# Optimization experiments

Hardware: AMD Instinct MI355X
Metric: run time of the kernel (lower is better)

The kernel has to match this reference:

```python
import jax, jax.numpy as jnp
import numpy as np

V, E, D = 100000, 128, 60  # vocab, embedding_size, d_alpha
B, J, M, P = 512, 101, 50, 5120
EPS = 1e-6


def setup_inputs() -> dict:
    key = jax.random.key(0)
    ks = jax.random.split(key, 12)
    s = 0.5 / E
    inp = {
        'batch_titems': jax.random.randint(ks[0], (B, J), 0, V),
        'batch_citems': jax.random.randint(ks[1], (B, M), 0, V),
        'batch_pad_ids': jax.random.randint(ks[2], (2, P), 0, M),
        't_emb': jax.random.uniform(ks[3], (V, E), jnp.float32, -s, s),
        'c_emb': jax.random.uniform(ks[4], (V, E), jnp.float32, -s, s),
        'Ac_w': jax.random.normal(ks[5], (D, E), jnp.float32) * 0.05,
        'Ac_b': jnp.zeros((D,), jnp.float32),
        'At_w': jax.random.normal(ks[6], (D, E), jnp.float32) * 0.05,
        'At_b': jnp.zeros((D,), jnp.float32),
        'Bc_w': jax.random.normal(ks[7], (E, E), jnp.float32) * 0.05,
        'Bc_b': jnp.zeros((E,), jnp.float32),
        'R_w': jax.random.normal(ks[8], (E, E), jnp.float32) * 0.05,
        'R_b': jnp.zeros((E,), jnp.float32),
    }
    return inp


def reference(batch_titems, batch_citems, batch_pad_ids, t_emb, c_emb,
              Ac_w, Ac_b, At_w, At_b, Bc_w, Bc_b, R_w, R_b):
    v = t_emb[batch_titems]            # [B, J, E] target item vectors
    u = c_emb[batch_citems]            # [B, M, E] context item vectors
    tp = v @ At_w.T + At_b             # [B, J, D]
    cp = u @ Ac_w.T + Ac_b             # [B, M, D]
    # cosine similarity with torch eps clamp on norms
    dot = jnp.einsum('bjd,bmd->bjm', tp, cp)
    nt = jnp.maximum(jnp.linalg.norm(tp, axis=-1), EPS)  # [B, J]
    nc = jnp.maximum(jnp.linalg.norm(cp, axis=-1), EPS)  # [B, M]
    cos = dot / (nt[:, :, None] * nc[:, None, :])        # [B, J, M]
    # pad mask: (batch, context-pos) pairs masked across all J target rows
    mask = jnp.zeros((cos.shape[0], cos.shape[2]), bool)
    mask = mask.at[batch_pad_ids[0], batch_pad_ids[1]].set(True)
    scores = jnp.where(mask[:, None, :], -jnp.inf, cos)
    attn = jax.nn.softmax(scores, axis=-1)               # [B, J, M]
    bu = u @ Bc_w.T + Bc_b                               # [B, M, E]
    alpha = jnp.einsum('bjm,bme->bje', attn, bu)         # [B, J, E]
    return alpha @ R_w.T + R_b                           # [B, J, E]
```

## Files before the change

### kernel.cpp

```cpp
#include <hip/hip_runtime.h>

typedef unsigned short u16;
typedef unsigned int   u32;
typedef short bf8 __attribute__((ext_vector_type(8)));
typedef float f4  __attribute__((ext_vector_type(4)));

#define NB   512
#define NJ   101
#define NM   50
#define NE   128
#define ND   60
#define NP   5120
#define NT   512
#define EPSV 1e-6f

#define T_B    0
#define C_B    16128
#define H_B    25344
#define NT2_B  43776
#define NC2_B  44224
#define MSK_B  44480
#define ARENA  44736

__device__ __forceinline__ u16 f2bh(float f) {
    return (u16)((__float_as_uint(f) + 0x8000u) >> 16);
}
__device__ __forceinline__ u32 pk2(float a, float b) {
    u32 ia = __float_as_uint(a) + 0x8000u;
    u32 ib = __float_as_uint(b) + 0x8000u;
    return (ia >> 16) | (ib & 0xFFFF0000u);
}
__device__ __forceinline__ bf8 pkfrag(float4 x, float4 y) {
    union { u32 u[4]; bf8 v; } r;
    r.u[0] = pk2(x.x, x.y); r.u[1] = pk2(x.z, x.w);
    r.u[2] = pk2(y.x, y.y); r.u[3] = pk2(y.z, y.w);
    return r.v;
}

__global__ __launch_bounds__(128) void w2_kernel(
    const float* __restrict__ Bc_w, const float* __restrict__ Bc_b,
    const float* __restrict__ R_w,  const float* __restrict__ R_b,
    const float* __restrict__ At_w, const float* __restrict__ Ac_w,
    u16* __restrict__ w2t, float* __restrict__ rb2,
    u16* __restrict__ atw, u16* __restrict__ acw)
{
    const int e = blockIdx.x, k = threadIdx.x;
    const float* Rrow = R_w + e * NE;
    float a0 = 0.f, a1 = 0.f, a2 = 0.f, a3 = 0.f;
    #pragma unroll 8
    for (int j = 0; j < NE; j += 4) {
        a0 += Rrow[j]     * Bc_w[j * NE + k];
        a1 += Rrow[j + 1] * Bc_w[(j + 1) * NE + k];
        a2 += Rrow[j + 2] * Bc_w[(j + 2) * NE + k];
        a3 += Rrow[j + 3] * Bc_w[(j + 3) * NE + k];
    }
    w2t[e * NE + k] = f2bh((a0 + a1) + (a2 + a3));
    if (e < ND) {
        atw[e * NE + k] = f2bh(At_w[e * NE + k]);
        acw[e * NE + k] = f2bh(Ac_w[e * NE + k]);
    }
    float c = Bc_b[k] * Rrow[k];
    for (int o = 32; o; o >>= 1) c += __shfl_xor(c, o, 64);
    __shared__ float part[2];
    if ((k & 63) == 0) part[k >> 6] = c;
    __syncthreads();
    if (k == 0) rb2[e] = part[0] + part[1] + R_b[e];
}

__device__ __forceinline__ void tp_full(int jt, int l15, int quad, const bf8* A,
    const u16* __restrict__ atw, const float* __restrict__ At_b,
    u16* __restrict__ tp16, float* __restrict__ nt2)
{
    #pragma unroll
    for (int dt = 0; dt < 4; dt++) {
        const int d = dt * 16 + l15;
        const u16* arow = atw + (size_t)((d < ND) ? d : 0) * NE;
        float bv = (d < ND) ? At_b[d] : 0.f;
        f4 acc = {bv, bv, bv, bv};
        #pragma unroll
        for (int ks = 0; ks < 4; ks++)
            acc = __builtin_amdgcn_mfma_f32_16x16x32_bf16(
                A[ks], *(const bf8*)(arow + ks * 32 + quad * 8), acc, 0, 0, 0);
        const int j0 = jt * 16 + quad * 4;
        #pragma unroll
        for (int r = 0; r < 4; r++) {
            float v = acc[r];
            tp16[(j0 + r) * 72 + d] = (d < ND) ? f2bh(v) : (u16)0;
            float q = (d < ND) ? v * v : 0.f;
            q += __shfl_xor(q, 1, 64); q += __shfl_xor(q, 2, 64);
            q += __shfl_xor(q, 4, 64); q += __shfl_xor(q, 8, 64);
            if (l15 == 0) atomicAdd(&nt2[j0 + r], q);
        }
    }
}

__device__ __forceinline__ void cp_full(int mt, int l15, int quad, const bf8* Au,
    const u16* __restrict__ acw, const float* __restrict__ Ac_b,
    u16* __restrict__ cp16, float* __restrict__ nc2)
{
    #pragma unroll
    for (int dt = 0; dt < 4; dt++) {
        const int d = dt * 16 + l15;
        const u16* arow = acw + (size_t)((d < ND) ? d : 0) * NE;
        float bv = (d < ND) ? Ac_b[d] : 0.f;
        f4 acc = {bv, bv, bv, bv};
        #pragma unroll
        for (int ks = 0; ks < 4; ks++)
            acc = __builtin_amdgcn_mfma_f32_16x16x32_bf16(
                Au[ks], *(const bf8*)(arow + ks * 32 + quad * 8), acc, 0, 0, 0);
        const int m0 = mt * 16 + quad * 4;
        #pragma unroll
        for (int r = 0; r < 4; r++) {
            float v = acc[r];
            cp16[(m0 + r) * 72 + d] = (d < ND) ? f2bh(v) : (u16)0;
            float q = (d < ND) ? v * v : 0.f;
            q += __shfl_xor(q, 1, 64); q += __shfl_xor(q, 2, 64);
            q += __shfl_xor(q, 4, 64); q += __shfl_xor(q, 8, 64);
            if (l15 == 0) atomicAdd(&nc2[m0 + r], q);
        }
    }
}

__device__ __forceinline__ void ht_group(int mtg, int l15, int quad, const bf8* Au,
    const u16* __restrict__ w2t, u16* __restrict__ hT16)
{
    #pragma unroll
    for (int et = 0; et < 8; et++) {
        const u16* wrow = w2t + (size_t)(et * 16 + l15) * NE;
        f4 acc = {0.f, 0.f, 0.f, 0.f};
        #pragma unroll
        for (int ks = 0; ks < 4; ks++)
            acc = __builtin_amdgcn_mfma_f32_16x16x32_bf16(
                *(const bf8*)(wrow + ks * 32 + quad * 8), Au[ks], acc, 0, 0, 0);
        const int e0 = et * 16 + quad * 4;
        #pragma unroll
        for (int r = 0; r < 4; r++)
            hT16[(e0 + r) * 72 + mtg * 16 + l15] = f2bh(acc[r]);
    }
}

__global__ __launch_bounds__(NT, 3) void aitv_kernel(
    const int* __restrict__ titems, const int* __restrict__ citems,
    const int* __restrict__ pad_ids,
    const float* __restrict__ t_emb, const float* __restrict__ c_emb,
    const u16* __restrict__ atw,     const float* __restrict__ At_b,
    const u16* __restrict__ acw,     const float* __restrict__ Ac_b,
    const u16* __restrict__ w2t,     const float* __restrict__ rb2g,
    float* __restrict__ out)
{
    const int b    = blockIdx.x;
    const int t    = threadIdx.x;
    const int wid  = t >> 6;
    const int lane = t & 63;
    const int l15  = lane & 15;
    const int quad = lane >> 4;

    __shared__ __align__(16) char arena[ARENA];
    u16*   tp16 = (u16*)(arena + T_B);   u16* at16 = (u16*)(arena + T_B);
    u16*   cp16 = (u16*)(arena + C_B);
    u16*   hT16 = (u16*)(arena + H_B);
    float* nt2  = (float*)(arena + NT2_B);
    float* nc2  = (float*)(arena + NC2_B);
    int*   msk  = (int*)(arena + MSK_B);

    float4 pxT[8];
    if (wid < 7) {
        int j = wid * 16 + l15; if (j > NJ - 1) j = NJ - 1;
        const float* vr = t_emb + (size_t)titems[b * NJ + j] * NE + quad * 8;
        #pragma unroll
        for (int h = 0; h < 8; h++)
            pxT[h] = *(const float4*)(vr + (h >> 1) * 32 + (h & 1) * 4);
    }
    const int mtu = (wid < 4) ? wid : wid - 4;
    int mrow = mtu * 16 + l15; if (mrow > NM - 1) mrow = NM - 1;
    const float* vrU = c_emb + (size_t)citems[b * NM + mrow] * NE + quad * 8;

    if (t < 112) nt2[t] = 0.f;
    else if (t < 176) nc2[t - 112] = 0.f;
    else if (t < 240) msk[t - 176] = 0;
    __syncthreads();

    float4 pxU[8];
    #pragma unroll
    for (int h = 0; h < 8; h++)
        pxU[h] = *(const float4*)(vrU + (h >> 1) * 32 + (h & 1) * 4);

    for (int i = t; i < NP; i += NT)
        if (pad_ids[i] == b) msk[pad_ids[NP + i]] = 1;

    bf8 At[4];
    if (wid < 7) {
        #pragma unroll
        for (int ks = 0; ks < 4; ks++) At[ks] = pkfrag(pxT[2 * ks], pxT[2 * ks + 1]);
        tp_full(wid, l15, quad, At, atw, At_b, tp16, nt2);
    }
    bf8 Au[4];
    #pragma unroll
    for (int ks = 0; ks < 4; ks++) Au[ks] = pkfrag(pxU[2 * ks], pxU[2 * ks + 1]);
    if (wid < 4) ht_group(mtu, l15, quad, Au, w2t, hT16);
    else         cp_full(mtu, l15, quad, Au, acw, Ac_b, cp16, nc2);
    __syncthreads();

    if (wid < 7) {
        const int jt = wid;
        f4 S[4];
        #pragma unroll
        for (int mt = 0; mt < 4; mt++) {
            f4 acc = {0.f, 0.f, 0.f, 0.f};
            #pragma unroll
            for (int ks = 0; ks < 2; ks++) {
                bf8 a  = *(const bf8*)(tp16 + (jt * 16 + l15) * 72 + ks * 32 + quad * 8);
                bf8 bb = *(const bf8*)(cp16 + (mt * 16 + l15) * 72 + ks * 32 + quad * 8);
                acc = __builtin_amdgcn_mfma_f32_16x16x32_bf16(a, bb, acc, 0, 0, 0);
            }
            S[mt] = acc;
        }
        bool valid[4]; float ncS[4];
        #pragma unroll
        for (int mt = 0; mt < 4; mt++) {
            int m = mt * 16 + l15;
            valid[mt] = (m < NM) && (msk[m] == 0);
            ncS[mt]   = valid[mt] ? fmaxf(sqrtf(nc2[m]), EPSV) : 1.f;
        }
        #pragma unroll
        for (int r = 0; r < 4; r++) {
            int j = jt * 16 + quad * 4 + r;
            float ntj = fmaxf(sqrtf(nt2[j]), EPSV);
            float x[4], mx = -INFINITY;
            #pragma unroll
            for (int mt = 0; mt < 4; mt++) {
                x[mt] = valid[mt] ? S[mt][r] / (ntj * ncS[mt]) : -INFINITY;
                mx = fmaxf(mx, x[mt]);
            }
            mx = fmaxf(mx, __shfl_xor(mx, 1, 64)); mx = fmaxf(mx, __shfl_xor(mx, 2, 64));
            mx = fmaxf(mx, __shfl_xor(mx, 4, 64)); mx = fmaxf(mx, __shfl_xor(mx, 8, 64));
            float p[4], sm = 0.f;
            #pragma unroll
            for (int mt = 0; mt < 4; mt++) {
                p[mt] = valid[mt] ? __expf(x[mt] - mx) : 0.f;
                sm += p[mt];
            }
            sm += __shfl_xor(sm, 1, 64); sm += __shfl_xor(sm, 2, 64);
            sm += __shfl_xor(sm, 4, 64); sm += __shfl_xor(sm, 8, 64);
            float inv = (sm > 0.f) ? 1.f / sm : 0.f;
            #pragma unroll
            for (int mt = 0; mt < 4; mt++)
                at16[j * 72 + mt * 16 + l15] = f2bh(p[mt] * inv);
        }
    }
    __syncthreads();

    for (int u = wid; u < 56; u += 8) {
        int jt = u >> 3, et = u & 7;
        float bv = rb2g[et * 16 + l15];
        f4 acc = {bv, bv, bv, bv};
        #pragma unroll
        for (int ks = 0; ks < 2; ks++) {
            bf8 a  = *(const bf8*)(at16 + (jt * 16 + l15) * 72 + ks * 32 + quad * 8);
            bf8 bb = *(const bf8*)(hT16 + (et * 16 + l15) * 72 + ks * 32 + quad * 8);
            acc = __builtin_amdgcn_mfma_f32_16x16x32_bf16(a, bb, acc, 0, 0, 0);
        }
        int e = et * 16 + l15, j0 = jt * 16 + quad * 4;
        #pragma unroll
        for (int r = 0; r < 4; r++) {
            int j = j0 + r;
            if (j < NJ) out[((size_t)b * NJ + j) * NE + e] = acc[r];
        }
    }
}

extern "C" void kernel_launch(void* const* d_in, const int* in_sizes, int n_in,
                              void* d_out, int out_size, void* d_ws, size_t ws_size,
                              hipStream_t stream) {
    const int*   titems  = (const int*)d_in[0];
    const int*   citems  = (const int*)d_in[1];
    const int*   pad_ids = (const int*)d_in[2];
    const float* t_emb   = (const float*)d_in[3];
    const float* c_emb   = (const float*)d_in[4];
    const float* Ac_w    = (const float*)d_in[5];
    const float* Ac_b    = (const float*)d_in[6];
    const float* At_w    = (const float*)d_in[7];
    const float* At_b    = (const float*)d_in[8];
    const float* Bc_w    = (const float*)d_in[9];
    const float* Bc_b    = (const float*)d_in[10];
    const float* R_w     = (const float*)d_in[11];
    const float* R_b     = (const float*)d_in[12];
    float* out = (float*)d_out;

    u16*   w2t = (u16*)d_ws;
    float* rb2 = (float*)((char*)d_ws + 32768);
    u16*   atw = (u16*)((char*)d_ws + 33280);
    u16*   acw = (u16*)((char*)d_ws + 48640);

    w2_kernel<<<NE, NE, 0, stream>>>(Bc_w, Bc_b, R_w, R_b, At_w, Ac_w,
                                     w2t, rb2, atw, acw);
    aitv_kernel<<<NB, NT, 0, stream>>>(titems, citems, pad_ids, t_emb, c_emb,
                                       atw, At_b, acw, Ac_b, w2t, rb2, out);
}
```

Baseline: 172.2 us.

## Split each batch row across two blocks by target-row halves

Launches two blocks per batch element, each handling half of the target-row tiles (4 and 3 tiles of 16 rows), and shrinks the LDS arena so more blocks fit per CU (launch bounds raised to 4 blocks). The aim is more parallelism and occupancy across the GPU's CUs. In exchange, each block redundantly gathers the context embeddings and recomputes cp, the hT projection and the pad mask, which doubles that part of the work and its memory traffic.

Result: slower. 197.7 us (+14.8%).

```diff
diff --git a/kernel.cpp b/kernel.cpp
--- a/kernel.cpp
+++ b/kernel.cpp
@@ -15,12 +15,12 @@
 #define EPSV 1e-6f
 
 #define T_B    0
-#define C_B    16128
-#define H_B    25344
-#define NT2_B  43776
-#define NC2_B  44224
-#define MSK_B  44480
-#define ARENA  44736
+#define C_B    9216
+#define H_B    18432
+#define NT2_B  36864
+#define NC2_B  37120
+#define MSK_B  37376
+#define ARENA  37632
 
 __device__ __forceinline__ u16 f2bh(float f) {
     return (u16)((__float_as_uint(f) + 0x8000u) >> 16);
@@ -67,7 +67,7 @@
     if (k == 0) rb2[e] = part[0] + part[1] + R_b[e];
 }
 
-__device__ __forceinline__ void tp_full(int jt, int l15, int quad, const bf8* A,
+__device__ __forceinline__ void tp_full(int ljt, int l15, int quad, const bf8* A,
     const u16* __restrict__ atw, const float* __restrict__ At_b,
     u16* __restrict__ tp16, float* __restrict__ nt2)
 {
@@ -81,7 +81,7 @@
         for (int ks = 0; ks < 4; ks++)
             acc = __builtin_amdgcn_mfma_f32_16x16x32_bf16(
                 A[ks], *(const bf8*)(arow + ks * 32 + quad * 8), acc, 0, 0, 0);
-        const int j0 = jt * 16 + quad * 4;
+        const int j0 = ljt * 16 + quad * 4;
         #pragma unroll
         for (int r = 0; r < 4; r++) {
             float v = acc[r];
@@ -139,7 +139,7 @@
     }
 }
 
-__global__ __launch_bounds__(NT, 3) void aitv_kernel(
+__global__ __launch_bounds__(NT, 4) void aitv_kernel(
     const int* __restrict__ titems, const int* __restrict__ citems,
     const int* __restrict__ pad_ids,
     const float* __restrict__ t_emb, const float* __restrict__ c_emb,
@@ -148,7 +148,10 @@
     const u16* __restrict__ w2t,     const float* __restrict__ rb2g,
     float* __restrict__ out)
 {
-    const int b    = blockIdx.x;
+    const int b    = blockIdx.x >> 1;
+    const int half = blockIdx.x & 1;
+    const int njh  = half ? 3 : 4;
+    const int jt0  = half * 4;
     const int t    = threadIdx.x;
     const int wid  = t >> 6;
     const int lane = t & 63;
@@ -164,20 +167,20 @@
     int*   msk  = (int*)(arena + MSK_B);
 
     float4 pxT[8];
-    if (wid < 7) {
-        int j = wid * 16 + l15; if (j > NJ - 1) j = NJ - 1;
+    if (wid < njh) {
+        int j = (jt0 + wid) * 16 + l15; if (j > NJ - 1) j = NJ - 1;
         const float* vr = t_emb + (size_t)titems[b * NJ + j] * NE + quad * 8;
         #pragma unroll
         for (int h = 0; h < 8; h++)
             pxT[h] = *(const float4*)(vr + (h >> 1) * 32 + (h & 1) * 4);
     }
-    const int mtu = (wid < 4) ? wid : wid - 4;
+    const int mtu = wid & 3;
     int mrow = mtu * 16 + l15; if (mrow > NM - 1) mrow = NM - 1;
     const float* vrU = c_emb + (size_t)citems[b * NM + mrow] * NE + quad * 8;
 
-    if (t < 112) nt2[t] = 0.f;
-    else if (t < 176) nc2[t - 112] = 0.f;
-    else if (t < 240) msk[t - 176] = 0;
+    if (t < 64) nt2[t] = 0.f;
+    else if (t < 128) nc2[t - 64] = 0.f;
+    else if (t < 192) msk[t - 128] = 0;
     __syncthreads();
 
     float4 pxU[8];
@@ -189,7 +192,7 @@
         if (pad_ids[i] == b) msk[pad_ids[NP + i]] = 1;
 
     bf8 At[4];
-    if (wid < 7) {
+    if (wid < njh) {
         #pragma unroll
         for (int ks = 0; ks < 4; ks++) At[ks] = pkfrag(pxT[2 * ks], pxT[2 * ks + 1]);
         tp_full(wid, l15, quad, At, atw, At_b, tp16, nt2);
@@ -201,15 +204,15 @@
     else         cp_full(mtu, l15, quad, Au, acw, Ac_b, cp16, nc2);
     __syncthreads();
 
-    if (wid < 7) {
-        const int jt = wid;
+    if (wid < njh) {
+        const int ljt = wid;
         f4 S[4];
         #pragma unroll
         for (int mt = 0; mt < 4; mt++) {
             f4 acc = {0.f, 0.f, 0.f, 0.f};
             #pragma unroll
             for (int ks = 0; ks < 2; ks++) {
-                bf8 a  = *(const bf8*)(tp16 + (jt * 16 + l15) * 72 + ks * 32 + quad * 8);
+                bf8 a  = *(const bf8*)(tp16 + (ljt * 16 + l15) * 72 + ks * 32 + quad * 8);
                 bf8 bb = *(const bf8*)(cp16 + (mt * 16 + l15) * 72 + ks * 32 + quad * 8);
                 acc = __builtin_amdgcn_mfma_f32_16x16x32_bf16(a, bb, acc, 0, 0, 0);
             }
@@ -224,8 +227,8 @@
         }
         #pragma unroll
         for (int r = 0; r < 4; r++) {
-            int j = jt * 16 + quad * 4 + r;
-            float ntj = fmaxf(sqrtf(nt2[j]), EPSV);
+            int lj = ljt * 16 + quad * 4 + r;
+            float ntj = fmaxf(sqrtf(nt2[lj]), EPSV);
             float x[4], mx = -INFINITY;
             #pragma unroll
             for (int mt = 0; mt < 4; mt++) {
@@ -245,22 +248,22 @@
             float inv = (sm > 0.f) ? 1.f / sm : 0.f;
             #pragma unroll
             for (int mt = 0; mt < 4; mt++)
-                at16[j * 72 + mt * 16 + l15] = f2bh(p[mt] * inv);
+                at16[lj * 72 + mt * 16 + l15] = f2bh(p[mt] * inv);
         }
     }
     __syncthreads();
 
-    for (int u = wid; u < 56; u += 8) {
-        int jt = u >> 3, et = u & 7;
+    for (int u = wid; u < njh * 8; u += 8) {
+        int ljt = u >> 3, et = u & 7;
         float bv = rb2g[et * 16 + l15];
         f4 acc = {bv, bv, bv, bv};
         #pragma unroll
         for (int ks = 0; ks < 2; ks++) {
-            bf8 a  = *(const bf8*)(at16 + (jt * 16 + l15) * 72 + ks * 32 + quad * 8);
+            bf8 a  = *(const bf8*)(at16 + (ljt * 16 + l15) * 72 + ks * 32 + quad * 8);
             bf8 bb = *(const bf8*)(hT16 + (et * 16 + l15) * 72 + ks * 32 + quad * 8);
             acc = __builtin_amdgcn_mfma_f32_16x16x32_bf16(a, bb, acc, 0, 0, 0);
         }
-        int e = et * 16 + l15, j0 = jt * 16 + quad * 4;
+        int e = et * 16 + l15, j0 = (jt0 + ljt) * 16 + quad * 4;
         #pragma unroll
         for (int r = 0; r < 4; r++) {
             int j = j0 + r;
@@ -294,6 +297,6 @@
 
     w2_kernel<<<NE, NE, 0, stream>>>(Bc_w, Bc_b, R_w, R_b, At_w, Ac_w,
                                      w2t, rb2, atw, acw);
-    aitv_kernel<<<NB, NT, 0, stream>>>(titems, citems, pad_ids, t_emb, c_emb,
-                                       atw, At_b, acw, Ac_b, w2t, rb2, out);
-}
+    aitv_kernel<<<2 * NB, NT, 0, stream>>>(titems, citems, pad_ids, t_emb, c_emb,
+                                           atw, At_b, acw, Ac_b, w2t, rb2, out);
+}
```
